# Performance work log

Measured on AMD Instinct MI355X. Metric: run time of the kernel, lower is better.

## Reference

```python
import jax, jax.numpy as jnp
import numpy as np

B, T, C, H = 2, 2048, 2048, 16
D = C // H  # head_dim = 128
SCALE = 1.0 / np.sqrt(D)


def setup_inputs() -> dict:
    key = jax.random.key(0)
    ks = jax.random.split(key, 9)
    x = jax.random.normal(ks[0], (B, T, C), dtype=jnp.float32)
    # additive causal mask [T, T]
    attn_mask = jnp.where(jnp.tril(jnp.ones((T, T), dtype=bool)), 0.0, -1e9).astype(jnp.float32)
    s_cc = 1.0 / np.sqrt(C)
    s_cd = 1.0 / np.sqrt(C)
    Wq = jax.random.normal(ks[1], (C, C), dtype=jnp.float32) * s_cc
    Wk = jax.random.normal(ks[2], (D, C), dtype=jnp.float32) * s_cd
    Wv = jax.random.normal(ks[3], (D, C), dtype=jnp.float32) * s_cd
    Wo = jax.random.normal(ks[4], (C, C), dtype=jnp.float32) * s_cc
    bq = jnp.zeros((C,), jnp.float32)
    bk = jnp.zeros((D,), jnp.float32)
    bv = jnp.zeros((D,), jnp.float32)
    bo = jnp.zeros((C,), jnp.float32)
    return {"x": x, "attn_mask": attn_mask, "Wq": Wq, "bq": bq, "Wk": Wk,
            "bk": bk, "Wv": Wv, "bv": bv, "Wo": Wo, "bo": bo}


def reference(x, attn_mask, Wq, bq, Wk, bk, Wv, bv, Wo, bo):
    # projections (torch Linear: x @ W.T + b)
    q = (x @ Wq.T + bq).reshape(B, T, H, D).transpose(0, 2, 1, 3)  # [B,H,T,D]
    k = x @ Wk.T + bk                                              # [B,T,D] single KV head
    v = x @ Wv.T + bv                                              # [B,T,D]
    # scores: broadcast shared K over all H query heads
    scores = jnp.einsum('bhtd,bsd->bhts', q, k) * SCALE            # [B,H,T,T]
    scores = scores + attn_mask  # [T,T] broadcasts over B,H
    attn = jax.nn.softmax(scores, axis=-1)
    out = jnp.einsum('bhts,bsd->bhtd', attn, v)                    # [B,H,T,D]
    out = out.transpose(0, 2, 1, 3).reshape(B, T, C)
    return out @ Wo.T + bo
```

## Files before the change

kernel.cpp:

```cpp
#include <hip/hip_runtime.h>
#include <stdint.h>

typedef unsigned short u16;
typedef __attribute__((ext_vector_type(8))) __bf16 bf16x8;
typedef __attribute__((ext_vector_type(4))) __bf16 bf16x4;
typedef __attribute__((ext_vector_type(4))) float f32x4;
typedef __attribute__((ext_vector_type(8))) u16 u16x8;
typedef __attribute__((ext_vector_type(4))) short s16x4;
typedef __attribute__((ext_vector_type(2))) unsigned int u32x2;

#define B_SZ 2
#define T_SZ 2048
#define C_SZ 2048
#define H_SZ 16
#define D_SZ 128
#define NQKV 2304
#define ATT_SCALE 0.08838834764831845f
#define LOG2E_SCALE 0.12751744f
#define DEFER_THR 90.50967f

typedef __attribute__((address_space(1))) void* as1_void_p;
typedef __attribute__((address_space(3))) void* as3_void_p;

__device__ __forceinline__ u16 f2b(float f) {
  union { float f; uint32_t u; } c; c.f = f;
  return (u16)((c.u + 0x7FFFu + ((c.u >> 16) & 1u)) >> 16);
}

__device__ __forceinline__ void gload_lds16(const u16* g, u16* l) {
  __builtin_amdgcn_global_load_lds((as1_void_p)g, (as3_void_p)l, 16, 0, 0);
}

__device__ __forceinline__ f32x4 mfma16(s16x4 a, s16x4 b, f32x4 c) {
#if __has_builtin(__builtin_amdgcn_mfma_f32_16x16x16bf16_1k)
  return __builtin_amdgcn_mfma_f32_16x16x16bf16_1k(a, b, c, 0, 0, 0);
#elif __has_builtin(__builtin_amdgcn_mfma_f32_16x16x16_bf16)
  return __builtin_amdgcn_mfma_f32_16x16x16_bf16(
      __builtin_bit_cast(bf16x4, a), __builtin_bit_cast(bf16x4, b), c, 0, 0, 0);
#else
  u32x2 ua = __builtin_bit_cast(u32x2, a);
  u32x2 ub = __builtin_bit_cast(u32x2, b);
  asm("s_nop 1\n\tv_mfma_f32_16x16x16_bf16 %0, %1, %2, %0\n\ts_nop 7"
      : "+v"(c) : "v"(ua), "v"(ub));
  return c;
#endif
}

__global__ __launch_bounds__(256) void cast_to_bf16(const float* __restrict__ in,
                                                    u16* __restrict__ out, int n) {
  int idx = (blockIdx.x * 256 + threadIdx.x) * 4;
  if (idx >= n) return;
  float4 f = *(const float4*)&in[idx];
  ushort4 o4;
  o4.x = f2b(f.x); o4.y = f2b(f.y); o4.z = f2b(f.z); o4.w = f2b(f.w);
  *(ushort4*)&out[idx] = o4;
}

__global__ __launch_bounds__(256) void build_bias(const float* __restrict__ bq,
                                                  const float* __restrict__ bk,
                                                  const float* __restrict__ bv,
                                                  float* __restrict__ out) {
  int i = blockIdx.x * 256 + threadIdx.x;
  if (i < C_SZ) out[i] = bq[i];
  else if (i < C_SZ + D_SZ) out[i] = bk[i - C_SZ];
  else if (i < NQKV) out[i] = bv[i - C_SZ - D_SZ];
}

template <typename OutT>
__global__ __launch_bounds__(256) void gemm_bt(const u16* __restrict__ A,
                                               const u16* __restrict__ Bm,
                                               const float* __restrict__ bias,
                                               OutT* __restrict__ C,
                                               int K, int ldc) {
  __shared__ u16 lsA[2][128 * 32];
  __shared__ u16 lsB[2][128 * 32];
  const int tid = threadIdx.x;
  const int lane = tid & 63;
  const int wave = tid >> 6;
  const int wr = wave >> 1, wc = wave & 1;
  const int l16 = lane & 15, lq = lane >> 4;
  const int brow = blockIdx.y * 128;
  const int bcol = blockIdx.x * 128;

  f32x4 acc[4][4] = {};

  auto STAGE = [&](int k0, int bs) {
#pragma unroll
    for (int i = 0; i < 2; i++) {
      const int woff = (i * 4 + wave) * 512;
      const int eoff = woff + lane * 8;
      const int r = eoff >> 5, c = eoff & 31;
      gload_lds16(A + (size_t)(brow + r) * K + k0 + c, &lsA[bs][woff]);
      gload_lds16(Bm + (size_t)(bcol + r) * K + k0 + c, &lsB[bs][woff]);
    }
  };

  STAGE(0, 0);
  __syncthreads();
  int cur = 0;
  for (int k0 = 0; k0 < K; k0 += 32) {
    if (k0 + 32 < K) STAGE(k0 + 32, cur ^ 1);

    bf16x8 af[4], bfr[4];
#pragma unroll
    for (int mi = 0; mi < 4; mi++)
      af[mi] = *(const bf16x8*)&lsA[cur][(wr * 64 + mi * 16 + l16) * 32 + lq * 8];
#pragma unroll
    for (int ni = 0; ni < 4; ni++)
      bfr[ni] = *(const bf16x8*)&lsB[cur][(wc * 64 + ni * 16 + l16) * 32 + lq * 8];
#pragma unroll
    for (int mi = 0; mi < 4; mi++)
#pragma unroll
      for (int ni = 0; ni < 4; ni++)
        acc[mi][ni] = __builtin_amdgcn_mfma_f32_16x16x32_bf16(af[mi], bfr[ni], acc[mi][ni], 0, 0, 0);

    __syncthreads();
    cur ^= 1;
  }

#pragma unroll
  for (int mi = 0; mi < 4; mi++)
#pragma unroll
    for (int ni = 0; ni < 4; ni++) {
      const int col = bcol + wc * 64 + ni * 16 + l16;
      const float bb = bias ? bias[col] : 0.0f;
#pragma unroll
      for (int r = 0; r < 4; r++) {
        const int row = brow + wr * 64 + mi * 16 + lq * 4 + r;
        const float v = acc[mi][ni][r] + bb;
        if constexpr (sizeof(OutT) == 2) {
          ((u16*)C)[(size_t)row * ldc + col] = f2b(v);
        } else {
          ((float*)C)[(size_t)row * ldc + col] = v;
        }
      }
    }
}

__global__ __launch_bounds__(256) void transpose_v(const u16* __restrict__ qkv,
                                                   u16* __restrict__ vT) {
  __shared__ u16 tile[64 * 136];
  const int tid = threadIdx.x;
  const int t0 = blockIdx.x * 64;
  const int b = blockIdx.y;
#pragma unroll
  for (int i = 0; i < 4; i++) {
    int idx = (i * 256 + tid) * 8;
    int r = idx >> 7, c = idx & 127;
    u16x8 v = *(const u16x8*)&qkv[(size_t)(b * T_SZ + t0 + r) * NQKV + (C_SZ + D_SZ) + c];
    *(u16x8*)&tile[r * 136 + c] = v;
  }
  __syncthreads();
#pragma unroll
  for (int i = 0; i < 4; i++) {
    int idx = (i * 256 + tid) * 8;
    int d = idx >> 6, t = idx & 63;
    u16x8 v;
#pragma unroll
    for (int j = 0; j < 8; j++) v[j] = tile[(t + j) * 136 + d];
    *(u16x8*)&vT[(size_t)(b * D_SZ + d) * T_SZ + t0 + t] = v;
  }
}

template <bool MASK>
__device__ __forceinline__ void attn_tile64(
    const u16* lk, const u16* lv,
    const bf16x8 (&aq)[4], f32x4 (&o)[8], float& lp, float& m,
    int q_rel, int l16, int lq)
{
  f32x4 s[4] = {};
#pragma unroll
  for (int kk = 0; kk < 4; kk++) {
#pragma unroll
    for (int nb = 0; nb < 4; nb++) {
      const int row = nb * 16 + l16;
      const bf16x8 kf = *(const bf16x8*)&lk[row * 128 + (((kk * 4 + lq) ^ (row & 7)) << 3)];
      s[nb] = __builtin_amdgcn_mfma_f32_16x16x32_bf16(kf, aq[kk], s[nb], 0, 0, 0);
    }
  }
  if (MASK) {
#pragma unroll
    for (int nb = 0; nb < 4; nb++)
#pragma unroll
      for (int rr = 0; rr < 4; rr++)
        if (nb * 16 + lq * 4 + rr > q_rel) s[nb][rr] -= 1e9f;
  }
  float mx = s[0][0];
#pragma unroll
  for (int nb = 0; nb < 4; nb++)
#pragma unroll
    for (int rr = 0; rr < 4; rr++) mx = fmaxf(mx, s[nb][rr]);
  mx = fmaxf(mx, __shfl_xor(mx, 16, 64));
  mx = fmaxf(mx, __shfl_xor(mx, 32, 64));
  if (__any(mx > m + DEFER_THR)) {
    const float mnew = fmaxf(m, mx);
    const float alpha = exp2f((m - mnew) * LOG2E_SCALE);
    m = mnew;
    lp *= alpha;
#pragma unroll
    for (int nd = 0; nd < 8; nd++)
#pragma unroll
      for (int e = 0; e < 4; e++) o[nd][e] *= alpha;
  }
#pragma unroll
  for (int nb = 0; nb < 4; nb++) {
    s16x4 pb;
#pragma unroll
    for (int e = 0; e < 4; e++) {
      const float p = exp2f((s[nb][e] - m) * LOG2E_SCALE);
      lp += p;
      pb[e] = (short)f2b(p);
    }
#pragma unroll
    for (int nd = 0; nd < 8; nd++) {
      const int row = nd * 16 + l16;
      const s16x4 av = *(const s16x4*)&lv[row * 64 +
          ((((nb << 1) | (lq >> 1)) ^ (row & 7)) << 3) + ((lq & 1) << 2)];
      o[nd] = mfma16(av, pb, o[nd]);
    }
  }
}

__global__ __launch_bounds__(256, 2) void attn_fwd(const u16* __restrict__ qkv,
                                                   const u16* __restrict__ vT,
                                                   u16* __restrict__ out) {
  __shared__ u16 lsK[2][64 * 128];
  __shared__ u16 lsV[2][128 * 64];
  const int tid = threadIdx.x;
  const int w = tid >> 6, lane = tid & 63;
  const int l16 = lane & 15, lq = lane >> 4;
  const int qL = blockIdx.x;
  const int qH = 31 - qL;
  const int h = blockIdx.y;
  const int b = blockIdx.z;
  const int bT = b * T_SZ;

  bf16x8 aqL[4], aqH[4];
  {
    const size_t rL = (size_t)(bT + qL * 64 + w * 16 + l16) * NQKV + h * D_SZ;
    const size_t rH = (size_t)(bT + qH * 64 + w * 16 + l16) * NQKV + h * D_SZ;
#pragma unroll
    for (int kk = 0; kk < 4; kk++) {
      aqL[kk] = *(const bf16x8*)&qkv[rL + kk * 32 + lq * 8];
      aqH[kk] = *(const bf16x8*)&qkv[rH + kk * 32 + lq * 8];
    }
  }

  f32x4 oL[8] = {}, oH[8] = {};
  float lpL = 0.f, lpH = 0.f;
  float mL = -INFINITY, mH = -INFINITY;
  const int relDiag = w * 16 + l16;

  const u16* kp[4];
  const u16* vp[4];
#pragma unroll
  for (int j = 0; j < 4; j++) {
    const int rk = w * 16 + j * 4 + (lane >> 4);
    const int ck = (lane & 15) ^ (rk & 7);
    kp[j] = qkv + (size_t)(bT + rk) * NQKV + C_SZ + ck * 8;
    const int rv = w * 32 + j * 8 + (lane >> 3);
    const int cv = (lane & 7) ^ (rv & 7);
    vp[j] = vT + (size_t)(b * D_SZ + rv) * T_SZ + cv * 8;
  }

  auto STAGE = [&](int kt, int bufsel) {
    const size_t koff = (size_t)kt * (64 * NQKV);
    const int voff = kt * 64;
#pragma unroll
    for (int j = 0; j < 4; j++) {
      gload_lds16(kp[j] + koff, &lsK[bufsel][w * 2048 + j * 512]);
      gload_lds16(vp[j] + voff, &lsV[bufsel][w * 2048 + j * 512]);
    }
  };

  STAGE(0, 0);
  __syncthreads();
  int cur = 0;
  for (int kt = 0; kt <= qH; kt++) {
    if (kt < qH) STAGE(kt + 1, cur ^ 1);
    if (kt == qH)
      attn_tile64<true>(lsK[cur], lsV[cur], aqH, oH, lpH, mH, relDiag, l16, lq);
    else
      attn_tile64<false>(lsK[cur], lsV[cur], aqH, oH, lpH, mH, 0, l16, lq);
    if (kt == qL)
      attn_tile64<true>(lsK[cur], lsV[cur], aqL, oL, lpL, mL, relDiag, l16, lq);
    else if (kt < qL)
      attn_tile64<false>(lsK[cur], lsV[cur], aqL, oL, lpL, mL, 0, l16, lq);
    __syncthreads();
    cur ^= 1;
  }

  lpL += __shfl_xor(lpL, 16, 64); lpL += __shfl_xor(lpL, 32, 64);
  lpH += __shfl_xor(lpH, 16, 64); lpH += __shfl_xor(lpH, 32, 64);
  const float rL = __builtin_amdgcn_rcpf(lpL);
  const float rH = __builtin_amdgcn_rcpf(lpH);
  const size_t rowL = (size_t)(bT + qL * 64 + w * 16 + l16) * C_SZ + h * D_SZ;
  const size_t rowH = (size_t)(bT + qH * 64 + w * 16 + l16) * C_SZ + h * D_SZ;
#pragma unroll
  for (int nd = 0; nd < 8; nd++) {
    ushort4 sL, sH;
    sL.x = f2b(oL[nd][0] * rL); sL.y = f2b(oL[nd][1] * rL);
    sL.z = f2b(oL[nd][2] * rL); sL.w = f2b(oL[nd][3] * rL);
    sH.x = f2b(oH[nd][0] * rH); sH.y = f2b(oH[nd][1] * rH);
    sH.z = f2b(oH[nd][2] * rH); sH.w = f2b(oH[nd][3] * rH);
    *(ushort4*)&out[rowL + nd * 16 + lq * 4] = sL;
    *(ushort4*)&out[rowH + nd * 16 + lq * 4] = sH;
  }
}

extern "C" void kernel_launch(void* const* d_in, const int* in_sizes, int n_in,
                              void* d_out, int out_size, void* d_ws, size_t ws_size,
                              hipStream_t stream) {
  const float* x  = (const float*)d_in[0];
  const float* Wq = (const float*)d_in[2];
  const float* bq = (const float*)d_in[3];
  const float* Wk = (const float*)d_in[4];
  const float* bk = (const float*)d_in[5];
  const float* Wv = (const float*)d_in[6];
  const float* bv = (const float*)d_in[7];
  const float* Wo = (const float*)d_in[8];
  const float* bo = (const float*)d_in[9];
  float* out = (float*)d_out;

  char* ws = (char*)d_ws;
  if (ws_size < 71312384) return;
  u16* xb     = (u16*)(ws + 0);
  u16* wqkv   = (u16*)(ws + 16777216);
  u16* wob    = (u16*)(ws + 26214400);
  u16* qkv    = (u16*)(ws + 34603008);
  u16* vT     = (u16*)(ws + 53477376);
  u16* ao     = (u16*)(ws + 54525952);
  float* bqkv = (float*)(ws + 71303168);

  cast_to_bf16<<<8192, 256, 0, stream>>>(x, xb, 8388608);
  cast_to_bf16<<<4096, 256, 0, stream>>>(Wq, wqkv, 4194304);
  cast_to_bf16<<<256, 256, 0, stream>>>(Wk, wqkv + 4194304, 262144);
  cast_to_bf16<<<256, 256, 0, stream>>>(Wv, wqkv + 4456448, 262144);
  cast_to_bf16<<<4096, 256, 0, stream>>>(Wo, wob, 4194304);
  build_bias<<<9, 256, 0, stream>>>(bq, bk, bv, bqkv);

  gemm_bt<u16><<<dim3(18, 32), 256, 0, stream>>>(xb, wqkv, bqkv, qkv, 2048, NQKV);
  transpose_v<<<dim3(32, 2), 256, 0, stream>>>(qkv, vT);
  attn_fwd<<<dim3(16, 16, 2), 256, 0, stream>>>(qkv, vT, ao);
  gemm_bt<float><<<dim3(16, 32), 256, 0, stream>>>(ao, wob, bo, out, 2048, 2048);
}
```

Baseline: 228.0 us.

## Single-buffer LDS with register prefetch to raise attention occupancy to 3 blocks

Replaces the double-buffered direct global-to-LDS loads with a single LDS buffer per K/V tile. The next tile is prefetched into registers during compute and written to LDS after a barrier. Halving LDS use lets launch bounds go from 2 to 3 blocks per CU, for more latency hiding. The cost is an extra barrier per iteration, extra VGPRs for the prefetch registers, and loss of the async LDS-load path.

```diff
diff --git a/kernel.cpp b/kernel.cpp
--- a/kernel.cpp
+++ b/kernel.cpp
@@ -221,11 +221,11 @@
   }
 }
 
-__global__ __launch_bounds__(256, 2) void attn_fwd(const u16* __restrict__ qkv,
+__global__ __launch_bounds__(256, 3) void attn_fwd(const u16* __restrict__ qkv,
                                                    const u16* __restrict__ vT,
                                                    u16* __restrict__ out) {
-  __shared__ u16 lsK[2][64 * 128];
-  __shared__ u16 lsV[2][128 * 64];
+  __shared__ u16 lsK[64 * 128];
+  __shared__ u16 lsV[128 * 64];
   const int tid = threadIdx.x;
   const int w = tid >> 6, lane = tid & 63;
   const int l16 = lane & 15, lq = lane >> 4;
@@ -251,43 +251,55 @@
   float mL = -INFINITY, mH = -INFINITY;
   const int relDiag = w * 16 + l16;
 
-  const u16* kp[4];
-  const u16* vp[4];
+  const int rk0 = w * 16 + (lane >> 4);
+  const int rv0 = w * 32 + (lane >> 3);
+  const u16* kbase = qkv + (size_t)(bT + rk0) * NQKV + C_SZ + (lane & 15) * 8;
+  const u16* vbase = vT + (size_t)(b * D_SZ + rv0) * T_SZ + (lane & 7) * 8;
+  int kdst[4], vdst[4];
 #pragma unroll
   for (int j = 0; j < 4; j++) {
-    const int rk = w * 16 + j * 4 + (lane >> 4);
-    const int ck = (lane & 15) ^ (rk & 7);
-    kp[j] = qkv + (size_t)(bT + rk) * NQKV + C_SZ + ck * 8;
-    const int rv = w * 32 + j * 8 + (lane >> 3);
-    const int cv = (lane & 7) ^ (rv & 7);
-    vp[j] = vT + (size_t)(b * D_SZ + rv) * T_SZ + cv * 8;
-  }
-
-  auto STAGE = [&](int kt, int bufsel) {
+    const int rk = rk0 + j * 4;
+    kdst[j] = rk * 128 + ((((lane & 15) ^ (rk & 7)) << 3));
+    const int rv = rv0 + j * 8;
+    vdst[j] = rv * 64 + ((((lane & 7) ^ (rv & 7)) << 3));
+  }
+
+  u16x8 kreg[4], vreg[4];
+  auto LOADREG = [&](int kt) {
     const size_t koff = (size_t)kt * (64 * NQKV);
     const int voff = kt * 64;
 #pragma unroll
     for (int j = 0; j < 4; j++) {
-      gload_lds16(kp[j] + koff, &lsK[bufsel][w * 2048 + j * 512]);
-      gload_lds16(vp[j] + voff, &lsV[bufsel][w * 2048 + j * 512]);
+      kreg[j] = *(const u16x8*)(kbase + koff + (size_t)j * (4 * NQKV));
+      vreg[j] = *(const u16x8*)(vbase + voff + j * (8 * T_SZ));
     }
   };
-
-  STAGE(0, 0);
+  auto WRITE = [&]() {
+#pragma unroll
+    for (int j = 0; j < 4; j++) {
+      *(u16x8*)&lsK[kdst[j]] = kreg[j];
+      *(u16x8*)&lsV[vdst[j]] = vreg[j];
+    }
+  };
+
+  LOADREG(0);
+  WRITE();
   __syncthreads();
-  int cur = 0;
   for (int kt = 0; kt <= qH; kt++) {
-    if (kt < qH) STAGE(kt + 1, cur ^ 1);
+    if (kt < qH) LOADREG(kt + 1);
     if (kt == qH)
-      attn_tile64<true>(lsK[cur], lsV[cur], aqH, oH, lpH, mH, relDiag, l16, lq);
+      attn_tile64<true>(lsK, lsV, aqH, oH, lpH, mH, relDiag, l16, lq);
     else
-      attn_tile64<false>(lsK[cur], lsV[cur], aqH, oH, lpH, mH, 0, l16, lq);
+      attn_tile64<false>(lsK, lsV, aqH, oH, lpH, mH, 0, l16, lq);
     if (kt == qL)
-      attn_tile64<true>(lsK[cur], lsV[cur], aqL, oL, lpL, mL, relDiag, l16, lq);
+      attn_tile64<true>(lsK, lsV, aqL, oL, lpL, mL, relDiag, l16, lq);
     else if (kt < qL)
-      attn_tile64<false>(lsK[cur], lsV[cur], aqL, oL, lpL, mL, 0, l16, lq);
+      attn_tile64<false>(lsK, lsV, aqL, oL, lpL, mL, 0, l16, lq);
     __syncthreads();
-    cur ^= 1;
+    if (kt < qH) {
+      WRITE();
+      __syncthreads();
+    }
   }
 
   lpL += __shfl_xor(lpL, 16, 64); lpL += __shfl_xor(lpL, 32, 64);
```

Result: slower. 376.3 us (+65.0%).

## Shrink attention KV tile to 32 with per-wave causal skipping; swizzle GEMM blocks

Applied to the files above, without the earlier changes.

The attention kernel now walks keys in 32-row tiles instead of 64. Each wave decides per tile whether to run the unmasked path, the masked path, or skip entirely, so fully masked work near the diagonal is no longer computed. Halving LDS use lets the kernel raise its occupancy hint to 4 blocks per CU. The trade-off is twice as many loop iterations and barriers. Separately, the GEMM remaps block indices in an interleaved order by groups of 8, aiming at better L2 locality across XCDs.

```diff
diff --git a/kernel.cpp b/kernel.cpp
--- a/kernel.cpp
+++ b/kernel.cpp
@@ -79,8 +79,11 @@
   const int wave = tid >> 6;
   const int wr = wave >> 1, wc = wave & 1;
   const int l16 = lane & 15, lq = lane >> 4;
-  const int brow = blockIdx.y * 128;
-  const int bcol = blockIdx.x * 128;
+  const int nwg = gridDim.x * gridDim.y;
+  int wg = blockIdx.y * gridDim.x + blockIdx.x;
+  wg = (wg & 7) * (nwg >> 3) + (wg >> 3);
+  const int brow = (wg / gridDim.x) * 128;
+  const int bcol = (wg % gridDim.x) * 128;
 
   f32x4 acc[4][4] = {};
 
@@ -163,16 +166,16 @@
 }
 
 template <bool MASK>
-__device__ __forceinline__ void attn_tile64(
+__device__ __forceinline__ void attn_tile32(
     const u16* lk, const u16* lv,
     const bf16x8 (&aq)[4], f32x4 (&o)[8], float& lp, float& m,
     int q_rel, int l16, int lq)
 {
-  f32x4 s[4] = {};
+  f32x4 s[2] = {};
 #pragma unroll
   for (int kk = 0; kk < 4; kk++) {
 #pragma unroll
-    for (int nb = 0; nb < 4; nb++) {
+    for (int nb = 0; nb < 2; nb++) {
       const int row = nb * 16 + l16;
       const bf16x8 kf = *(const bf16x8*)&lk[row * 128 + (((kk * 4 + lq) ^ (row & 7)) << 3)];
       s[nb] = __builtin_amdgcn_mfma_f32_16x16x32_bf16(kf, aq[kk], s[nb], 0, 0, 0);
@@ -180,16 +183,13 @@
   }
   if (MASK) {
 #pragma unroll
-    for (int nb = 0; nb < 4; nb++)
+    for (int nb = 0; nb < 2; nb++)
 #pragma unroll
       for (int rr = 0; rr < 4; rr++)
         if (nb * 16 + lq * 4 + rr > q_rel) s[nb][rr] -= 1e9f;
   }
-  float mx = s[0][0];
-#pragma unroll
-  for (int nb = 0; nb < 4; nb++)
-#pragma unroll
-    for (int rr = 0; rr < 4; rr++) mx = fmaxf(mx, s[nb][rr]);
+  float mx = fmaxf(fmaxf(fmaxf(s[0][0], s[0][1]), fmaxf(s[0][2], s[0][3])),
+                   fmaxf(fmaxf(s[1][0], s[1][1]), fmaxf(s[1][2], s[1][3])));
   mx = fmaxf(mx, __shfl_xor(mx, 16, 64));
   mx = fmaxf(mx, __shfl_xor(mx, 32, 64));
   if (__any(mx > m + DEFER_THR)) {
@@ -203,7 +203,7 @@
       for (int e = 0; e < 4; e++) o[nd][e] *= alpha;
   }
 #pragma unroll
-  for (int nb = 0; nb < 4; nb++) {
+  for (int nb = 0; nb < 2; nb++) {
     s16x4 pb;
 #pragma unroll
     for (int e = 0; e < 4; e++) {
@@ -214,18 +214,18 @@
 #pragma unroll
     for (int nd = 0; nd < 8; nd++) {
       const int row = nd * 16 + l16;
-      const s16x4 av = *(const s16x4*)&lv[row * 64 +
-          ((((nb << 1) | (lq >> 1)) ^ (row & 7)) << 3) + ((lq & 1) << 2)];
+      const s16x4 av = *(const s16x4*)&lv[row * 32 +
+          ((((nb << 1) | (lq >> 1)) ^ (row & 3)) << 3) + ((lq & 1) << 2)];
       o[nd] = mfma16(av, pb, o[nd]);
     }
   }
 }
 
-__global__ __launch_bounds__(256, 2) void attn_fwd(const u16* __restrict__ qkv,
+__global__ __launch_bounds__(256, 4) void attn_fwd(const u16* __restrict__ qkv,
                                                    const u16* __restrict__ vT,
                                                    u16* __restrict__ out) {
-  __shared__ u16 lsK[2][64 * 128];
-  __shared__ u16 lsV[2][128 * 64];
+  __shared__ u16 lsK[2][32 * 128];
+  __shared__ u16 lsV[2][128 * 32];
   const int tid = threadIdx.x;
   const int w = tid >> 6, lane = tid & 63;
   const int l16 = lane & 15, lq = lane >> 4;
@@ -249,43 +249,46 @@
   f32x4 oL[8] = {}, oH[8] = {};
   float lpL = 0.f, lpH = 0.f;
   float mL = -INFINITY, mH = -INFINITY;
-  const int relDiag = w * 16 + l16;
-
-  const u16* kp[4];
-  const u16* vp[4];
-#pragma unroll
-  for (int j = 0; j < 4; j++) {
-    const int rk = w * 16 + j * 4 + (lane >> 4);
-    const int ck = (lane & 15) ^ (rk & 7);
-    kp[j] = qkv + (size_t)(bT + rk) * NQKV + C_SZ + ck * 8;
-    const int rv = w * 32 + j * 8 + (lane >> 3);
-    const int cv = (lane & 7) ^ (rv & 7);
-    vp[j] = vT + (size_t)(b * D_SZ + rv) * T_SZ + cv * 8;
+  const int wqL = qL * 64 + w * 16;
+  const int wqH = qH * 64 + w * 16;
+
+  const u16* kp[2];
+  const u16* vp[2];
+#pragma unroll
+  for (int j = 0; j < 2; j++) {
+    const int rk = w * 8 + j * 4 + (lane >> 4);
+    const int sck = (lane & 15) ^ (rk & 7);
+    kp[j] = qkv + (size_t)(bT + rk) * NQKV + C_SZ + sck * 8;
+    const int rv = w * 32 + j * 16 + (lane >> 2);
+    const int scv = (lane & 3) ^ (rv & 3);
+    vp[j] = vT + (size_t)(b * D_SZ + rv) * T_SZ + scv * 8;
   }
 
   auto STAGE = [&](int kt, int bufsel) {
-    const size_t koff = (size_t)kt * (64 * NQKV);
-    const int voff = kt * 64;
-#pragma unroll
-    for (int j = 0; j < 4; j++) {
-      gload_lds16(kp[j] + koff, &lsK[bufsel][w * 2048 + j * 512]);
-      gload_lds16(vp[j] + voff, &lsV[bufsel][w * 2048 + j * 512]);
+    const size_t koff = (size_t)kt * (32 * NQKV);
+    const int voff = kt * 32;
+#pragma unroll
+    for (int j = 0; j < 2; j++) {
+      gload_lds16(kp[j] + koff, &lsK[bufsel][(w * 128 + j * 64) * 8]);
+      gload_lds16(vp[j] + voff, &lsV[bufsel][(w * 128 + j * 64) * 8]);
     }
   };
 
+  const int nkt = 2 * qH + 2;
   STAGE(0, 0);
   __syncthreads();
   int cur = 0;
-  for (int kt = 0; kt <= qH; kt++) {
-    if (kt < qH) STAGE(kt + 1, cur ^ 1);
-    if (kt == qH)
-      attn_tile64<true>(lsK[cur], lsV[cur], aqH, oH, lpH, mH, relDiag, l16, lq);
-    else
-      attn_tile64<false>(lsK[cur], lsV[cur], aqH, oH, lpH, mH, 0, l16, lq);
-    if (kt == qL)
-      attn_tile64<true>(lsK[cur], lsV[cur], aqL, oL, lpL, mL, relDiag, l16, lq);
-    else if (kt < qL)
-      attn_tile64<false>(lsK[cur], lsV[cur], aqL, oL, lpL, mL, 0, l16, lq);
+  for (int kt = 0; kt < nkt; kt++) {
+    const int kv0 = kt << 5;
+    if (kt + 1 < nkt) STAGE(kt + 1, cur ^ 1);
+    if (kv0 + 31 <= wqH)
+      attn_tile32<false>(lsK[cur], lsV[cur], aqH, oH, lpH, mH, 0, l16, lq);
+    else if (kv0 <= wqH + 15)
+      attn_tile32<true>(lsK[cur], lsV[cur], aqH, oH, lpH, mH, wqH + l16 - kv0, l16, lq);
+    if (kv0 + 31 <= wqL)
+      attn_tile32<false>(lsK[cur], lsV[cur], aqL, oL, lpL, mL, 0, l16, lq);
+    else if (kv0 <= wqL + 15)
+      attn_tile32<true>(lsK[cur], lsV[cur], aqL, oL, lpL, mL, wqL + l16 - kv0, l16, lq);
     __syncthreads();
     cur ^= 1;
   }
@@ -294,8 +297,8 @@
   lpH += __shfl_xor(lpH, 16, 64); lpH += __shfl_xor(lpH, 32, 64);
   const float rL = __builtin_amdgcn_rcpf(lpL);
   const float rH = __builtin_amdgcn_rcpf(lpH);
-  const size_t rowL = (size_t)(bT + qL * 64 + w * 16 + l16) * C_SZ + h * D_SZ;
-  const size_t rowH = (size_t)(bT + qH * 64 + w * 16 + l16) * C_SZ + h * D_SZ;
+  const size_t rowL = (size_t)(bT + wqL + l16) * C_SZ + h * D_SZ;
+  const size_t rowH = (size_t)(bT + wqH + l16) * C_SZ + h * D_SZ;
 #pragma unroll
   for (int nd = 0; nd < 8; nd++) {
     ushort4 sL, sH;
```

Result: slower. 282.3 us (+23.8%).
